# Kernel tuning notes

Hardware: AMD Instinct MI355X
Metric: run time of the kernel (lower is better)

## Reference

```python
import jax, jax.numpy as jnp
import numpy as np

NUM_CLASSES = 21
THRESH = 0.5
VAR = (0.1, 0.2)
B, P, O = 128, 8732, 16

def setup_inputs() -> dict:
    key = jax.random.key(0)
    ks = jax.random.split(key, 7)
    loc_preds = jax.random.normal(ks[0], (B, P, 4), jnp.float32)
    score_preds = jax.random.normal(ks[1], (B, P, NUM_CLASSES), jnp.float32)
    # priors in center-size form (cx, cy, w, h)
    pc = jax.random.uniform(ks[2], (P, 2), minval=0.05, maxval=0.95)
    pwh = jax.random.uniform(ks[3], (P, 2), minval=0.05, maxval=0.4)
    priors = jnp.concatenate([pc, pwh], axis=1).astype(jnp.float32)
    # ground truth: valid point-form boxes + label in last column
    gc = jax.random.uniform(ks[4], (B, O, 2), minval=0.2, maxval=0.8)
    gwh = jax.random.uniform(ks[5], (B, O, 2), minval=0.05, maxval=0.3)
    boxes = jnp.concatenate([gc - gwh / 2, gc + gwh / 2], axis=-1)
    labels = jax.random.randint(ks[6], (B, O, 1), 1, NUM_CLASSES).astype(jnp.float32)
    gt_data = jnp.concatenate([boxes, labels], axis=-1).astype(jnp.float32)
    return {"loc_preds": loc_preds, "score_preds": score_preds,
            "gt_data": gt_data, "priors": priors}

def _iou(a, b):
    # a: (O,4) point form, b: (P,4) point form -> (O,P)
    lt = jnp.maximum(a[:, None, :2], b[None, :, :2])
    rb = jnp.minimum(a[:, None, 2:], b[None, :, 2:])
    wh = jnp.clip(rb - lt, 0.0)
    inter = wh[..., 0] * wh[..., 1]
    area_a = (a[:, 2] - a[:, 0]) * (a[:, 3] - a[:, 1])
    area_b = (b[:, 2] - b[:, 0]) * (b[:, 3] - b[:, 1])
    return inter / (area_a[:, None] + area_b[None, :] - inter)

def _encode(matched, priors):
    # matched: (P,4) point form; priors: (P,4) center-size form
    g_c = (matched[:, :2] + matched[:, 2:]) / 2 - priors[:, :2]
    g_c = g_c / (VAR[0] * priors[:, 2:])
    g_wh = (matched[:, 2:] - matched[:, :2]) / priors[:, 2:]
    g_wh = jnp.log(g_wh) / VAR[1]
    return jnp.concatenate([g_c, g_wh], axis=1)

def _match_one(gt_loc, gt_cls, priors_pt, priors):
    ious = _iou(gt_loc, priors_pt)                    # (O, P)
    best_prior_idx = jnp.argmax(ious, axis=1)         # (O,)
    best_truth_overlap = jnp.max(ious, axis=0)        # (P,)
    best_truth_idx = jnp.argmax(ious, axis=0)         # (P,)
    # ensure every gt's best prior is kept positive and assigned to that gt
    best_truth_overlap = best_truth_overlap.at[best_prior_idx].set(2.0)
    best_truth_idx = best_truth_idx.at[best_prior_idx].set(jnp.arange(gt_loc.shape[0]))
    matched = gt_loc[best_truth_idx]                  # (P, 4)
    conf = gt_cls[best_truth_idx]
    conf = jnp.where(best_truth_overlap < THRESH, 0.0, conf)
    return _encode(matched, priors), conf.astype(jnp.int32)

def reference(loc_preds, score_preds, gt_data, priors):
    priors_pt = jnp.concatenate([priors[:, :2] - priors[:, 2:] / 2,
                                 priors[:, :2] + priors[:, 2:] / 2], axis=1)
    gt_loc, gt_cls = gt_data[..., :4], gt_data[..., 4]
    loc_targets, score_targets = jax.vmap(
        lambda l, c: _match_one(l, c, priors_pt, priors))(gt_loc, gt_cls)
    pos = score_targets > 0                           # (B, P)
    num_matched = jnp.sum(pos).astype(jnp.float32)

    # SmoothL1 over positive boxes (sum reduction)
    d = jnp.abs(loc_preds - loc_targets)
    sl1 = jnp.where(d < 1.0, 0.5 * d * d, d - 0.5)    # (B, P, 4)
    loc_loss = jnp.sum(jnp.where(pos[..., None], sl1, 0.0))

    # per-box cross-entropy on all boxes
    lse = jax.nn.logsumexp(score_preds, axis=-1)      # (B, P)
    gathered = jnp.take_along_axis(score_preds, score_targets[..., None],
                                   axis=-1)[..., 0]
    ce = lse - gathered                               # (B, P)

    # hard negative mining via double argsort ranking
    mine = jnp.where(pos, 0.0, ce)
    idx = jnp.argsort(-mine, axis=1)
    rank = jnp.argsort(idx, axis=1)
    num_pos = jnp.sum(pos, axis=1)                    # (B,)
    total_pos = jnp.sum(num_pos)
    num_neg = jnp.minimum(3 * num_pos, P - total_pos - 1)
    neg = rank < num_neg[:, None]

    sel = pos | neg
    conf_loss = jnp.sum(jnp.where(sel, ce, 0.0))
    return loc_loss / num_matched, conf_loss / num_matched
```

## Files before the change

### kernel.cpp

```cpp
#include <hip/hip_runtime.h>
#include <cstdint>
#include <cstddef>

#define B 128
#define P 8732
#define NC 21
#define O 16
#define THRESH 0.5f
#define NB1 8
#define NBX2 4
#define BPB 2304
#define WPW 576
#define NPART (B * NBX2)
#define SLABF 1536

typedef unsigned long long u64;
typedef unsigned int u32;
typedef unsigned char u8;

__device__ __forceinline__ float iou_pt(float a0, float a1, float a2, float a3,
                                        float b0, float b1, float b2, float b3) {
    float ltx = fmaxf(a0, b0), lty = fmaxf(a1, b1);
    float rbx = fminf(a2, b2), rby = fminf(a3, b3);
    float wx = fmaxf(rbx - ltx, 0.0f), wy = fmaxf(rby - lty, 0.0f);
    float inter = wx * wy;
    float aa = (a2 - a0) * (a3 - a1);
    float ab = (b2 - b0) * (b3 - b1);
    return inter / (aa + ab - inter);
}

__global__ void __launch_bounds__(256) k_pass1(const float* __restrict__ gt,
                                               const float* __restrict__ priors,
                                               u64* __restrict__ bk,
                                               u8* __restrict__ bidx) {
    const int b = blockIdx.y;
    __shared__ float s_gt[O * 4];
    __shared__ u64 s_wk[4][O];
    const int tid = threadIdx.x;
    const int wave = tid >> 6, lane = tid & 63;
    if (tid < O * 4) {
        int o = tid >> 2, c = tid & 3;
        s_gt[tid] = gt[(b * O + o) * 5 + c];
    }
    __syncthreads();

    u64 lk[O];
#pragma unroll
    for (int o = 0; o < O; o++) lk[o] = 0ull;

    for (int p = blockIdx.x * 256 + tid; p < P; p += NB1 * 256) {
        float4 pr = reinterpret_cast<const float4*>(priors)[p];
        float b0 = pr.x - pr.z * 0.5f, b1 = pr.y - pr.w * 0.5f;
        float b2 = pr.x + pr.z * 0.5f, b3 = pr.y + pr.w * 0.5f;
        float bov = -1.0f; int bo = 0;
#pragma unroll
        for (int o = 0; o < O; o++) {
            float v = iou_pt(s_gt[o * 4 + 0], s_gt[o * 4 + 1], s_gt[o * 4 + 2], s_gt[o * 4 + 3],
                             b0, b1, b2, b3);
            u64 key = ((u64)__float_as_uint(v) << 32) | (u64)(0xFFFFFFFFu - (u32)p);
            lk[o] = (key > lk[o]) ? key : lk[o];
            if (v > bov) { bov = v; bo = o; }
        }
        bidx[(size_t)b * P + p] = (u8)(bo | ((bov >= THRESH) ? 0x80 : 0));
    }

#pragma unroll
    for (int o = 0; o < O; o++) {
        u64 k = lk[o];
#pragma unroll
        for (int off = 32; off > 0; off >>= 1) {
            u64 other = (u64)__shfl_xor((long long)k, off, 64);
            k = (other > k) ? other : k;
        }
        if (lane == 0) s_wk[wave][o] = k;
    }
    __syncthreads();
    if (tid < O) {
        u64 k = s_wk[0][tid];
#pragma unroll
        for (int w = 1; w < 4; w++) { u64 v = s_wk[w][tid]; k = (v > k) ? v : k; }
        bk[((size_t)b * O + tid) * NB1 + blockIdx.x] = k;
    }
}

__device__ __forceinline__ void stage64(const float* __restrict__ gsrc,
                                        float* lds, int nf4, int lane) {
    const char* src = (const char*)gsrc;
    char* dst = (char*)lds;
#pragma unroll
    for (int i = 0; i < 6; i++) {
        int idx = i * 64 + lane;
        if (idx >= nf4) idx = nf4 - 1;
        __builtin_amdgcn_global_load_lds(
            (const __attribute__((address_space(1))) u32*)(src + (size_t)idx * 16),
            (__attribute__((address_space(3))) u32*)(dst + i * 1024),
            16, 0, 0);
    }
}

__global__ void __launch_bounds__(256) k_pass2(const float* __restrict__ gt,
                                               const float* __restrict__ priors,
                                               const u64* __restrict__ bk,
                                               const u8* __restrict__ bidx,
                                               const float* __restrict__ loc_preds,
                                               const float* __restrict__ scores,
                                               float* __restrict__ mine,
                                               double* __restrict__ pl,
                                               double* __restrict__ pc,
                                               int* __restrict__ pn) {
    const int b = blockIdx.y;
    const int tid = threadIdx.x;
    const int wave = tid >> 6, lane = tid & 63;
    __shared__ float s_slab[4][3][SLABF];
    __shared__ float s_gt[O * 5];
    __shared__ int s_bp[O];

    if (tid < O * 5) s_gt[tid] = gt[b * O * 5 + tid];
    if (tid < O) {
        u64 k = bk[((size_t)b * O + tid) * NB1];
#pragma unroll
        for (int i = 1; i < NB1; i++) {
            u64 v = bk[((size_t)b * O + tid) * NB1 + i];
            k = (v > k) ? v : k;
        }
        s_bp[tid] = (int)(0xFFFFFFFFu - (u32)(k & 0xFFFFFFFFull));
    }
    __syncthreads();

    const int wbase = blockIdx.x * BPB + wave * WPW;
    int wp = P - wbase; if (wp > WPW) wp = WPW;
    const int nchunk = (wp > 0) ? ((wp + 63) >> 6) : 0;

    float l_loc = 0.f, l_ce = 0.f;
    int l_np = 0;

    if (nchunk > 0) {
        for (int c0 = 0; c0 < 3 && c0 < nchunk; ++c0) {
            int nv0 = wp - c0 * 64; if (nv0 > 64) nv0 = 64;
            stage64(scores + ((size_t)b * P + wbase + c0 * 64) * NC,
                    &s_slab[wave][c0][0], nv0 * 21 / 4, lane);
        }
        for (int c = 0; c < nchunk; ++c) {
            const int base = wbase + c * 64;
            int nv = wp - c * 64; if (nv > 64) nv = 64;

            int ahead = nchunk - 1 - c; if (ahead > 2) ahead = 2;
            if (ahead == 2)      asm volatile("s_waitcnt vmcnt(12)" ::: "memory");
            else if (ahead == 1) asm volatile("s_waitcnt vmcnt(6)" ::: "memory");
            else                 asm volatile("s_waitcnt vmcnt(0)" ::: "memory");
            __builtin_amdgcn_sched_barrier(0);

            if (lane < nv) {
                const int p = base + lane;
                const float* fsl = &s_slab[wave][c % 3][lane * NC];
                float fs[NC];
#pragma unroll
                for (int cc = 0; cc < NC; cc++) fs[cc] = fsl[cc];

                int e = (int)bidx[(size_t)b * P + p];
                int best_idx = e & 0x3F;
                bool matched = (e & 0x80) != 0;
#pragma unroll
                for (int o = 0; o < O; o++) {
                    if (s_bp[o] == p) { best_idx = o; matched = true; }
                }
                int cls = matched ? (int)s_gt[best_idx * 5 + 4] : 0;

                float mx = fs[0];
#pragma unroll
                for (int cc = 1; cc < NC; cc++) mx = fmaxf(mx, fs[cc]);
                float se = 0.0f;
#pragma unroll
                for (int cc = 0; cc < NC; cc++) se += __expf(fs[cc] - mx);
                float lse = mx + __logf(se);
                float g = fs[0];
#pragma unroll
                for (int cc = 1; cc < NC; cc++) g = (cc == cls) ? fs[cc] : g;
                float ce = lse - g;

                mine[(size_t)b * P + p] = matched ? 0.0f : ce;

                if (matched) {
                    l_np++;
                    l_ce += ce;
                    float4 pr = reinterpret_cast<const float4*>(priors)[p];
                    float m0 = s_gt[best_idx * 5 + 0], m1 = s_gt[best_idx * 5 + 1];
                    float m2 = s_gt[best_idx * 5 + 2], m3 = s_gt[best_idx * 5 + 3];
                    float tx = ((m0 + m2) * 0.5f - pr.x) / (0.1f * pr.z);
                    float ty = ((m1 + m3) * 0.5f - pr.y) / (0.1f * pr.w);
                    float tw = __logf((m2 - m0) / pr.z) * 5.0f;
                    float th = __logf((m3 - m1) / pr.w) * 5.0f;
                    float4 lp = reinterpret_cast<const float4*>(loc_preds)[(size_t)b * P + p];
                    float d0 = fabsf(lp.x - tx), d1 = fabsf(lp.y - ty);
                    float d2 = fabsf(lp.z - tw), d3 = fabsf(lp.w - th);
                    float s0 = d0 < 1.0f ? 0.5f * d0 * d0 : d0 - 0.5f;
                    float s1 = d1 < 1.0f ? 0.5f * d1 * d1 : d1 - 0.5f;
                    float s2 = d2 < 1.0f ? 0.5f * d2 * d2 : d2 - 0.5f;
                    float s3 = d3 < 1.0f ? 0.5f * d3 * d3 : d3 - 0.5f;
                    l_loc += (s0 + s1) + (s2 + s3);
                }
            }

            if (c + 3 < nchunk) {
                int nv3 = wp - (c + 3) * 64; if (nv3 > 64) nv3 = 64;
                asm volatile("s_waitcnt lgkmcnt(0)" ::: "memory");
                stage64(scores + ((size_t)b * P + base + 3 * 64) * NC,
                        &s_slab[wave][c % 3][0], nv3 * 21 / 4, lane);
            }
        }
    }

#pragma unroll
    for (int off = 32; off > 0; off >>= 1) {
        l_loc += __shfl_xor(l_loc, off, 64);
        l_ce  += __shfl_xor(l_ce, off, 64);
        l_np  += __shfl_xor(l_np, off, 64);
    }
    __shared__ double s_loc[4], s_ce[4];
    __shared__ int s_np[4];
    if (lane == 0) { s_loc[wave] = (double)l_loc; s_ce[wave] = (double)l_ce; s_np[wave] = l_np; }
    __syncthreads();
    if (tid == 0) {
        int q = b * NBX2 + blockIdx.x;
        pl[q] = (s_loc[0] + s_loc[1]) + (s_loc[2] + s_loc[3]);
        pc[q] = (s_ce[0] + s_ce[1]) + (s_ce[2] + s_ce[3]);
        pn[q] = s_np[0] + s_np[1] + s_np[2] + s_np[3];
    }
}

__global__ void __launch_bounds__(1024) k_hardneg(const float* __restrict__ mine,
                                                  const int* __restrict__ pn,
                                                  double* __restrict__ pneg) {
    const int b = blockIdx.x;
    const int tid = threadIdx.x;
    const int lane = tid & 63, wave = tid >> 6;
    __shared__ float s_mine[P];
    __shared__ u32 s_hist[256];
    __shared__ u32 s_sel[2];
    __shared__ double s_red[16];
    __shared__ int s_ti[16];
    __shared__ int s_npx[NBX2];
    __shared__ int s_k;

    {
        int t = 0;
        for (int i = tid; i < NPART; i += 1024) t += pn[i];
#pragma unroll
        for (int off = 32; off > 0; off >>= 1) t += __shfl_xor(t, off, 64);
        if (lane == 0) s_ti[wave] = t;
    }
    if (tid < NBX2) s_npx[tid] = pn[b * NBX2 + tid];
    __syncthreads();
    if (tid == 0) {
        int tp = 0;
#pragma unroll
        for (int w = 0; w < 16; w++) tp += s_ti[w];
        int np = 0;
#pragma unroll
        for (int x = 0; x < NBX2; x++) np += s_npx[x];
        int k = 3 * np;
        int cap = P - tp - 1;
        if (cap < k) k = cap;
        s_k = k;
    }
    __syncthreads();
    const int k = s_k;

    if (k <= 0) {
        if (tid == 0) pneg[b] = 0.0;
        return;
    }

    for (int i = tid; i < P; i += 1024) s_mine[i] = mine[(size_t)b * P + i];
    if (tid == 0) { s_sel[0] = 0u; s_sel[1] = (u32)k; }
    __syncthreads();

    for (int shift = 24; shift >= 0; shift -= 8) {
        if (tid < 256) s_hist[tid] = 0u;
        __syncthreads();
        u32 prefix = s_sel[0];
        u32 kr = s_sel[1];
        u32 himask = (shift == 24) ? 0u : (0xFFFFFFFFu << (shift + 8));
        for (int i = tid; i < P; i += 1024) {
            u32 v = __float_as_uint(s_mine[i]);
            if ((v & himask) == prefix) atomicAdd(&s_hist[(v >> shift) & 255u], 1u);
        }
        __syncthreads();
        if (tid < 64) {
            const int L = tid;
            const int btop = 255 - 4 * L;
            u32 h0 = s_hist[btop], h1 = s_hist[btop - 1], h2 = s_hist[btop - 2], h3 = s_hist[btop - 3];
            u32 g4 = h0 + h1 + h2 + h3;
            u32 x = g4;
#pragma unroll
            for (int off = 1; off < 64; off <<= 1) {
                u32 v = __shfl_up(x, off, 64);
                if (L >= off) x += v;
            }
            u32 excl = x - g4;
            if (excl < kr && excl + g4 >= kr) {
                u32 c = excl; int chosen = btop; u32 kloc = kr;
                u32 nc;
                nc = c + h0; if (c < kr && nc >= kr) { chosen = btop;     kloc = kr - c; } c = nc;
                nc = c + h1; if (c < kr && nc >= kr) { chosen = btop - 1; kloc = kr - c; } c = nc;
                nc = c + h2; if (c < kr && nc >= kr) { chosen = btop - 2; kloc = kr - c; } c = nc;
                nc = c + h3; if (c < kr && nc >= kr) { chosen = btop - 3; kloc = kr - c; } c = nc;
                s_sel[0] = prefix | ((u32)chosen << shift);
                s_sel[1] = kloc;
            }
        }
        __syncthreads();
    }

    u32 tbits = s_sel[0];
    u32 kr = s_sel[1];
    float T = __uint_as_float(tbits);

    double sd = 0.0;
    for (int i = tid; i < P; i += 1024) {
        u32 v = __float_as_uint(s_mine[i]);
        if (v > tbits) sd += (double)s_mine[i];
    }
#pragma unroll
    for (int off = 32; off > 0; off >>= 1) sd += __shfl_xor(sd, off, 64);
    if (lane == 0) s_red[wave] = sd;
    __syncthreads();
    if (tid == 0) {
        double tt = 0.0;
#pragma unroll
        for (int w = 0; w < 16; w++) tt += s_red[w];
        pneg[b] = tt + (double)kr * (double)T;
    }
}

__global__ void __launch_bounds__(1024) k_fin(const double* __restrict__ pl,
                                              const double* __restrict__ pc,
                                              const int* __restrict__ pn,
                                              const double* __restrict__ pneg,
                                              float* __restrict__ out) {
    const int tid = threadIdx.x;
    const int lane = tid & 63, wave = tid >> 6;
    __shared__ double s_l[16], s_c[16], s_g[16];
    __shared__ int s_t[16];

    double tl = 0.0, tc = 0.0, tg = 0.0;
    int tn = 0;
    for (int i = tid; i < NPART; i += 1024) { tl += pl[i]; tc += pc[i]; tn += pn[i]; }
    if (tid < B) tg = pneg[tid];
#pragma unroll
    for (int off = 32; off > 0; off >>= 1) {
        tl += __shfl_xor(tl, off, 64);
        tc += __shfl_xor(tc, off, 64);
        tg += __shfl_xor(tg, off, 64);
        tn += __shfl_xor(tn, off, 64);
    }
    if (lane == 0) { s_l[wave] = tl; s_c[wave] = tc; s_g[wave] = tg; s_t[wave] = tn; }
    __syncthreads();
    if (tid == 0) {
        double al = 0.0, ac = 0.0, ag = 0.0;
        int an = 0;
#pragma unroll
        for (int w = 0; w < 16; w++) { al += s_l[w]; ac += s_c[w]; ag += s_g[w]; an += s_t[w]; }
        double n = (double)an;
        out[0] = (float)(al / n);
        out[1] = (float)((ac + ag) / n);
    }
}

extern "C" void kernel_launch(void* const* d_in, const int* in_sizes, int n_in,
                              void* d_out, int out_size, void* d_ws, size_t ws_size,
                              hipStream_t stream) {
    const float* loc_preds = (const float*)d_in[0];
    const float* scores    = (const float*)d_in[1];
    const float* gt        = (const float*)d_in[2];
    const float* priors    = (const float*)d_in[3];

    char* ws = (char*)d_ws;
    u64* bk      = (u64*)ws;
    double* pl   = (double*)(ws + 131072);
    double* pc   = (double*)(ws + 135168);
    int* pn      = (int*)(ws + 139264);
    double* pneg = (double*)(ws + 141312);
    u8* bidx     = (u8*)(ws + 142336);
    float* mine  = (float*)(ws + 1260032);


    k_pass1<<<dim3(NB1, B), dim3(256), 0, stream>>>(gt, priors, bk, bidx);
    k_pass2<<<dim3(NBX2, B), dim3(256), 0, stream>>>(
        gt, priors, bk, bidx, loc_preds, scores, mine, pl, pc, pn);
    k_hardneg<<<dim3(B), dim3(1024), 0, stream>>>(mine, pn, pneg);
    k_fin<<<dim3(1), dim3(1024), 0, stream>>>(pl, pc, pn, pneg, (float*)d_out);
}
```

Baseline: 60.99 us.

## Merge IoU matching and score streaming into one launch, fix positives separately

```diff
diff --git a/kernel.cpp b/kernel.cpp
--- a/kernel.cpp
+++ b/kernel.cpp
@@ -11,12 +11,15 @@
 #define NBX2 4
 #define BPB 2304
 #define WPW 576
-#define NPART (B * NBX2)
 #define SLABF 1536
+#define SCORE_BLKS (B * NBX2)
+#define P1_BLKS (B * NB1)
 
 typedef unsigned long long u64;
 typedef unsigned int u32;
 typedef unsigned char u8;
+
+#define VMW(n) asm volatile("s_waitcnt vmcnt(" #n ")" ::: "memory")
 
 __device__ __forceinline__ float iou_pt(float a0, float a1, float a2, float a3,
                                         float b0, float b1, float b2, float b3) {
@@ -29,60 +32,6 @@
     return inter / (aa + ab - inter);
 }
 
-__global__ void __launch_bounds__(256) k_pass1(const float* __restrict__ gt,
-                                               const float* __restrict__ priors,
-                                               u64* __restrict__ bk,
-                                               u8* __restrict__ bidx) {
-    const int b = blockIdx.y;
-    __shared__ float s_gt[O * 4];
-    __shared__ u64 s_wk[4][O];
-    const int tid = threadIdx.x;
-    const int wave = tid >> 6, lane = tid & 63;
-    if (tid < O * 4) {
-        int o = tid >> 2, c = tid & 3;
-        s_gt[tid] = gt[(b * O + o) * 5 + c];
-    }
-    __syncthreads();
-
-    u64 lk[O];
-#pragma unroll
-    for (int o = 0; o < O; o++) lk[o] = 0ull;
-
-    for (int p = blockIdx.x * 256 + tid; p < P; p += NB1 * 256) {
-        float4 pr = reinterpret_cast<const float4*>(priors)[p];
-        float b0 = pr.x - pr.z * 0.5f, b1 = pr.y - pr.w * 0.5f;
-        float b2 = pr.x + pr.z * 0.5f, b3 = pr.y + pr.w * 0.5f;
-        float bov = -1.0f; int bo = 0;
-#pragma unroll
-        for (int o = 0; o < O; o++) {
-            float v = iou_pt(s_gt[o * 4 + 0], s_gt[o * 4 + 1], s_gt[o * 4 + 2], s_gt[o * 4 + 3],
-                             b0, b1, b2, b3);
-            u64 key = ((u64)__float_as_uint(v) << 32) | (u64)(0xFFFFFFFFu - (u32)p);
-            lk[o] = (key > lk[o]) ? key : lk[o];
-            if (v > bov) { bov = v; bo = o; }
-        }
-        bidx[(size_t)b * P + p] = (u8)(bo | ((bov >= THRESH) ? 0x80 : 0));
-    }
-
-#pragma unroll
-    for (int o = 0; o < O; o++) {
-        u64 k = lk[o];
-#pragma unroll
-        for (int off = 32; off > 0; off >>= 1) {
-            u64 other = (u64)__shfl_xor((long long)k, off, 64);
-            k = (other > k) ? other : k;
-        }
-        if (lane == 0) s_wk[wave][o] = k;
-    }
-    __syncthreads();
-    if (tid < O) {
-        u64 k = s_wk[0][tid];
-#pragma unroll
-        for (int w = 1; w < 4; w++) { u64 v = s_wk[w][tid]; k = (v > k) ? v : k; }
-        bk[((size_t)b * O + tid) * NB1 + blockIdx.x] = k;
-    }
-}
-
 __device__ __forceinline__ void stage64(const float* __restrict__ gsrc,
                                         float* lds, int nf4, int lane) {
     const char* src = (const char*)gsrc;
@@ -98,73 +47,50 @@
     }
 }
 
-__global__ void __launch_bounds__(256) k_pass2(const float* __restrict__ gt,
-                                               const float* __restrict__ priors,
-                                               const u64* __restrict__ bk,
-                                               const u8* __restrict__ bidx,
-                                               const float* __restrict__ loc_preds,
-                                               const float* __restrict__ scores,
-                                               float* __restrict__ mine,
-                                               double* __restrict__ pl,
-                                               double* __restrict__ pc,
-                                               int* __restrict__ pn) {
-    const int b = blockIdx.y;
+__global__ void __launch_bounds__(256) k_main(const float* __restrict__ gt,
+                                              const float* __restrict__ priors,
+                                              const float* __restrict__ scores,
+                                              u64* __restrict__ bk,
+                                              u8* __restrict__ bidx,
+                                              float* __restrict__ mine) {
+    __shared__ union {
+        float slab[4][3][SLABF];
+        struct { u64 wk[4][O]; float gt4[O * 4]; } p1;
+    } sm;
     const int tid = threadIdx.x;
     const int wave = tid >> 6, lane = tid & 63;
-    __shared__ float s_slab[4][3][SLABF];
-    __shared__ float s_gt[O * 5];
-    __shared__ int s_bp[O];
-
-    if (tid < O * 5) s_gt[tid] = gt[b * O * 5 + tid];
-    if (tid < O) {
-        u64 k = bk[((size_t)b * O + tid) * NB1];
-#pragma unroll
-        for (int i = 1; i < NB1; i++) {
-            u64 v = bk[((size_t)b * O + tid) * NB1 + i];
-            k = (v > k) ? v : k;
-        }
-        s_bp[tid] = (int)(0xFFFFFFFFu - (u32)(k & 0xFFFFFFFFull));
-    }
-    __syncthreads();
-
-    const int wbase = blockIdx.x * BPB + wave * WPW;
-    int wp = P - wbase; if (wp > WPW) wp = WPW;
-    const int nchunk = (wp > 0) ? ((wp + 63) >> 6) : 0;
-
-    float l_loc = 0.f, l_ce = 0.f;
-    int l_np = 0;
-
-    if (nchunk > 0) {
+    const int bid = blockIdx.x;
+
+    if (bid < SCORE_BLKS) {
+        const int b = bid >> 2;
+        const int bx = bid & 3;
+        const int wbase = bx * BPB + wave * WPW;
+        int wp = P - wbase; if (wp > WPW) wp = WPW;
+        const int nchunk = (wp + 63) >> 6;
+
         for (int c0 = 0; c0 < 3 && c0 < nchunk; ++c0) {
             int nv0 = wp - c0 * 64; if (nv0 > 64) nv0 = 64;
             stage64(scores + ((size_t)b * P + wbase + c0 * 64) * NC,
-                    &s_slab[wave][c0][0], nv0 * 21 / 4, lane);
+                    &sm.slab[wave][c0][0], nv0 * 21 / 4, lane);
         }
         for (int c = 0; c < nchunk; ++c) {
             const int base = wbase + c * 64;
             int nv = wp - c * 64; if (nv > 64) nv = 64;
-
             int ahead = nchunk - 1 - c; if (ahead > 2) ahead = 2;
-            if (ahead == 2)      asm volatile("s_waitcnt vmcnt(12)" ::: "memory");
-            else if (ahead == 1) asm volatile("s_waitcnt vmcnt(6)" ::: "memory");
-            else                 asm volatile("s_waitcnt vmcnt(0)" ::: "memory");
+            if (ahead == 2) {
+                if (c == 0) VMW(12); else if (c == 1) VMW(13); else VMW(14);
+            } else if (ahead == 1) {
+                if (c == 0) VMW(6); else if (c == 1) VMW(7); else VMW(8);
+            } else {
+                VMW(0);
+            }
             __builtin_amdgcn_sched_barrier(0);
 
             if (lane < nv) {
-                const int p = base + lane;
-                const float* fsl = &s_slab[wave][c % 3][lane * NC];
+                const float* fsl = &sm.slab[wave][c % 3][lane * NC];
                 float fs[NC];
 #pragma unroll
                 for (int cc = 0; cc < NC; cc++) fs[cc] = fsl[cc];
-
-                int e = (int)bidx[(size_t)b * P + p];
-                int best_idx = e & 0x3F;
-                bool matched = (e & 0x80) != 0;
-#pragma unroll
-                for (int o = 0; o < O; o++) {
-                    if (s_bp[o] == p) { best_idx = o; matched = true; }
-                }
-                int cls = matched ? (int)s_gt[best_idx * 5 + 4] : 0;
 
                 float mx = fs[0];
 #pragma unroll
@@ -173,39 +99,151 @@
 #pragma unroll
                 for (int cc = 0; cc < NC; cc++) se += __expf(fs[cc] - mx);
                 float lse = mx + __logf(se);
-                float g = fs[0];
-#pragma unroll
-                for (int cc = 1; cc < NC; cc++) g = (cc == cls) ? fs[cc] : g;
-                float ce = lse - g;
-
-                mine[(size_t)b * P + p] = matched ? 0.0f : ce;
-
-                if (matched) {
-                    l_np++;
-                    l_ce += ce;
-                    float4 pr = reinterpret_cast<const float4*>(priors)[p];
-                    float m0 = s_gt[best_idx * 5 + 0], m1 = s_gt[best_idx * 5 + 1];
-                    float m2 = s_gt[best_idx * 5 + 2], m3 = s_gt[best_idx * 5 + 3];
-                    float tx = ((m0 + m2) * 0.5f - pr.x) / (0.1f * pr.z);
-                    float ty = ((m1 + m3) * 0.5f - pr.y) / (0.1f * pr.w);
-                    float tw = __logf((m2 - m0) / pr.z) * 5.0f;
-                    float th = __logf((m3 - m1) / pr.w) * 5.0f;
-                    float4 lp = reinterpret_cast<const float4*>(loc_preds)[(size_t)b * P + p];
-                    float d0 = fabsf(lp.x - tx), d1 = fabsf(lp.y - ty);
-                    float d2 = fabsf(lp.z - tw), d3 = fabsf(lp.w - th);
-                    float s0 = d0 < 1.0f ? 0.5f * d0 * d0 : d0 - 0.5f;
-                    float s1 = d1 < 1.0f ? 0.5f * d1 * d1 : d1 - 0.5f;
-                    float s2 = d2 < 1.0f ? 0.5f * d2 * d2 : d2 - 0.5f;
-                    float s3 = d3 < 1.0f ? 0.5f * d3 * d3 : d3 - 0.5f;
-                    l_loc += (s0 + s1) + (s2 + s3);
-                }
+                mine[(size_t)b * P + base + lane] = lse - fs[0];
             }
 
             if (c + 3 < nchunk) {
                 int nv3 = wp - (c + 3) * 64; if (nv3 > 64) nv3 = 64;
                 asm volatile("s_waitcnt lgkmcnt(0)" ::: "memory");
                 stage64(scores + ((size_t)b * P + base + 3 * 64) * NC,
-                        &s_slab[wave][c % 3][0], nv3 * 21 / 4, lane);
+                        &sm.slab[wave][c % 3][0], nv3 * 21 / 4, lane);
+            }
+        }
+    } else {
+        const int pid = bid - SCORE_BLKS;
+        const int bx = pid & 7;
+        const int b = pid >> 3;
+        if (tid < O * 4) {
+            int o = tid >> 2, c = tid & 3;
+            sm.p1.gt4[tid] = gt[(b * O + o) * 5 + c];
+        }
+        __syncthreads();
+
+        u64 lk[O];
+#pragma unroll
+        for (int o = 0; o < O; o++) lk[o] = 0ull;
+
+        for (int p = bx * 256 + tid; p < P; p += NB1 * 256) {
+            float4 pr = reinterpret_cast<const float4*>(priors)[p];
+            float b0 = pr.x - pr.z * 0.5f, b1 = pr.y - pr.w * 0.5f;
+            float b2 = pr.x + pr.z * 0.5f, b3 = pr.y + pr.w * 0.5f;
+            float bov = -1.0f; int bo = 0;
+#pragma unroll
+            for (int o = 0; o < O; o++) {
+                float v = iou_pt(sm.p1.gt4[o * 4 + 0], sm.p1.gt4[o * 4 + 1],
+                                 sm.p1.gt4[o * 4 + 2], sm.p1.gt4[o * 4 + 3],
+                                 b0, b1, b2, b3);
+                u64 key = ((u64)__float_as_uint(v) << 32) | (u64)(0xFFFFFFFFu - (u32)p);
+                lk[o] = (key > lk[o]) ? key : lk[o];
+                if (v > bov) { bov = v; bo = o; }
+            }
+            bidx[(size_t)b * P + p] = (u8)(bo | ((bov >= THRESH) ? 0x80 : 0));
+        }
+
+#pragma unroll
+        for (int o = 0; o < O; o++) {
+            u64 k = lk[o];
+#pragma unroll
+            for (int off = 32; off > 0; off >>= 1) {
+                u64 other = (u64)__shfl_xor((long long)k, off, 64);
+                k = (other > k) ? other : k;
+            }
+            if (lane == 0) sm.p1.wk[wave][o] = k;
+        }
+        __syncthreads();
+        if (tid < O) {
+            u64 k = sm.p1.wk[0][tid];
+#pragma unroll
+            for (int w = 1; w < 4; w++) { u64 v = sm.p1.wk[w][tid]; k = (v > k) ? v : k; }
+            bk[((size_t)b * O + tid) * NB1 + bx] = k;
+        }
+    }
+}
+
+__global__ void __launch_bounds__(256) k_fix(const float* __restrict__ gt,
+                                             const float* __restrict__ priors,
+                                             const float* __restrict__ loc_preds,
+                                             const float* __restrict__ scores,
+                                             const u64* __restrict__ bk,
+                                             const u8* __restrict__ bidx,
+                                             float* __restrict__ mine,
+                                             int* __restrict__ npA,
+                                             double* __restrict__ plA,
+                                             double* __restrict__ pcA,
+                                             double* __restrict__ acc,
+                                             u32* __restrict__ ticket) {
+    const int b = blockIdx.x;
+    const int tid = threadIdx.x;
+    const int lane = tid & 63, wave = tid >> 6;
+    __shared__ float s_gt[O * 5];
+    __shared__ int s_ovr[O];
+    __shared__ double s_l[4], s_c[4];
+    __shared__ int s_n[4];
+
+    if (b == 0 && tid == 0) { acc[0] = 0.0; *ticket = 0u; }
+    if (tid < O * 5) s_gt[tid] = gt[b * O * 5 + tid];
+    if (tid < O) {
+        u64 k = bk[((size_t)b * O + tid) * NB1];
+#pragma unroll
+        for (int i = 1; i < NB1; i++) {
+            u64 v = bk[((size_t)b * O + tid) * NB1 + i];
+            k = (v > k) ? v : k;
+        }
+        s_ovr[tid] = (int)(0xFFFFFFFFu - (u32)(k & 0xFFFFFFFFull));
+    }
+    __syncthreads();
+
+    float l_loc = 0.f, l_ce = 0.f;
+    int l_np = 0;
+
+    for (int i4 = tid; i4 < P / 4; i4 += 256) {
+        u32 w = *reinterpret_cast<const u32*>(bidx + (size_t)b * P + i4 * 4);
+#pragma unroll
+        for (int j = 0; j < 4; j++) {
+            const int p = i4 * 4 + j;
+            int e = (int)((w >> (8 * j)) & 0xFFu);
+#pragma unroll
+            for (int o = 0; o < O; o++)
+                if (s_ovr[o] == p) e = o | 0x80;
+            if (e & 0x80) {
+                int best_idx = e & 0x3F;
+                int cls = (int)s_gt[best_idx * 5 + 4];
+
+                const float* sp = scores + ((size_t)b * P + p) * NC;
+                float fs[NC];
+#pragma unroll
+                for (int cc = 0; cc < NC; cc++) fs[cc] = sp[cc];
+                float mx = fs[0];
+#pragma unroll
+                for (int cc = 1; cc < NC; cc++) mx = fmaxf(mx, fs[cc]);
+                float se = 0.0f;
+#pragma unroll
+                for (int cc = 0; cc < NC; cc++) se += __expf(fs[cc] - mx);
+                float lse = mx + __logf(se);
+                float g = fs[0];
+#pragma unroll
+                for (int cc = 1; cc < NC; cc++) g = (cc == cls) ? fs[cc] : g;
+                float ce = lse - g;
+
+                mine[(size_t)b * P + p] = 0.0f;
+                l_np++;
+                l_ce += ce;
+
+                float4 pr = reinterpret_cast<const float4*>(priors)[p];
+                float m0 = s_gt[best_idx * 5 + 0], m1 = s_gt[best_idx * 5 + 1];
+                float m2 = s_gt[best_idx * 5 + 2], m3 = s_gt[best_idx * 5 + 3];
+                float tx = ((m0 + m2) * 0.5f - pr.x) / (0.1f * pr.z);
+                float ty = ((m1 + m3) * 0.5f - pr.y) / (0.1f * pr.w);
+                float tw = __logf((m2 - m0) / pr.z) * 5.0f;
+                float th = __logf((m3 - m1) / pr.w) * 5.0f;
+                float4 lp = reinterpret_cast<const float4*>(loc_preds)[(size_t)b * P + p];
+                float d0 = fabsf(lp.x - tx), d1 = fabsf(lp.y - ty);
+                float d2 = fabsf(lp.z - tw), d3 = fabsf(lp.w - th);
+                float s0 = d0 < 1.0f ? 0.5f * d0 * d0 : d0 - 0.5f;
+                float s1 = d1 < 1.0f ? 0.5f * d1 * d1 : d1 - 0.5f;
+                float s2 = d2 < 1.0f ? 0.5f * d2 * d2 : d2 - 0.5f;
+                float s3 = d3 < 1.0f ? 0.5f * d3 * d3 : d3 - 0.5f;
+                l_loc += (s0 + s1) + (s2 + s3);
             }
         }
     }
@@ -216,21 +254,22 @@
         l_ce  += __shfl_xor(l_ce, off, 64);
         l_np  += __shfl_xor(l_np, off, 64);
     }
-    __shared__ double s_loc[4], s_ce[4];
-    __shared__ int s_np[4];
-    if (lane == 0) { s_loc[wave] = (double)l_loc; s_ce[wave] = (double)l_ce; s_np[wave] = l_np; }
+    if (lane == 0) { s_l[wave] = (double)l_loc; s_c[wave] = (double)l_ce; s_n[wave] = l_np; }
     __syncthreads();
     if (tid == 0) {
-        int q = b * NBX2 + blockIdx.x;
-        pl[q] = (s_loc[0] + s_loc[1]) + (s_loc[2] + s_loc[3]);
-        pc[q] = (s_ce[0] + s_ce[1]) + (s_ce[2] + s_ce[3]);
-        pn[q] = s_np[0] + s_np[1] + s_np[2] + s_np[3];
+        plA[b] = (s_l[0] + s_l[1]) + (s_l[2] + s_l[3]);
+        pcA[b] = (s_c[0] + s_c[1]) + (s_c[2] + s_c[3]);
+        npA[b] = s_n[0] + s_n[1] + s_n[2] + s_n[3];
     }
 }
 
 __global__ void __launch_bounds__(1024) k_hardneg(const float* __restrict__ mine,
-                                                  const int* __restrict__ pn,
-                                                  double* __restrict__ pneg) {
+                                                  const int* __restrict__ npA,
+                                                  const double* __restrict__ plA,
+                                                  const double* __restrict__ pcA,
+                                                  double* __restrict__ acc,
+                                                  u32* __restrict__ ticket,
+                                                  float* __restrict__ out) {
     const int b = blockIdx.x;
     const int tid = threadIdx.x;
     const int lane = tid & 63, wave = tid >> 6;
@@ -238,130 +277,95 @@
     __shared__ u32 s_hist[256];
     __shared__ u32 s_sel[2];
     __shared__ double s_red[16];
-    __shared__ int s_ti[16];
-    __shared__ int s_npx[NBX2];
-    __shared__ int s_k;
-
-    {
-        int t = 0;
-        for (int i = tid; i < NPART; i += 1024) t += pn[i];
-#pragma unroll
-        for (int off = 32; off > 0; off >>= 1) t += __shfl_xor(t, off, 64);
-        if (lane == 0) s_ti[wave] = t;
-    }
-    if (tid < NBX2) s_npx[tid] = pn[b * NBX2 + tid];
-    __syncthreads();
+    __shared__ int s_k, s_tp;
+
     if (tid == 0) {
         int tp = 0;
-#pragma unroll
-        for (int w = 0; w < 16; w++) tp += s_ti[w];
-        int np = 0;
-#pragma unroll
-        for (int x = 0; x < NBX2; x++) np += s_npx[x];
+        for (int i = 0; i < B; i++) tp += npA[i];
+        int np = npA[b];
         int k = 3 * np;
         int cap = P - tp - 1;
         if (cap < k) k = cap;
         s_k = k;
+        s_tp = tp;
     }
     __syncthreads();
     const int k = s_k;
 
-    if (k <= 0) {
-        if (tid == 0) pneg[b] = 0.0;
-        return;
-    }
-
-    for (int i = tid; i < P; i += 1024) s_mine[i] = mine[(size_t)b * P + i];
-    if (tid == 0) { s_sel[0] = 0u; s_sel[1] = (u32)k; }
-    __syncthreads();
-
-    for (int shift = 24; shift >= 0; shift -= 8) {
-        if (tid < 256) s_hist[tid] = 0u;
+    if (k > 0) {
+        for (int i = tid; i < P; i += 1024) s_mine[i] = mine[(size_t)b * P + i];
+        if (tid == 0) { s_sel[0] = 0u; s_sel[1] = (u32)k; }
         __syncthreads();
-        u32 prefix = s_sel[0];
+
+        for (int shift = 24; shift >= 0; shift -= 8) {
+            if (tid < 256) s_hist[tid] = 0u;
+            __syncthreads();
+            u32 prefix = s_sel[0];
+            u32 kr = s_sel[1];
+            u32 himask = (shift == 24) ? 0u : (0xFFFFFFFFu << (shift + 8));
+            for (int i = tid; i < P; i += 1024) {
+                u32 v = __float_as_uint(s_mine[i]);
+                if ((v & himask) == prefix) atomicAdd(&s_hist[(v >> shift) & 255u], 1u);
+            }
+            __syncthreads();
+            if (tid < 64) {
+                const int L = tid;
+                const int btop = 255 - 4 * L;
+                u32 h0 = s_hist[btop], h1 = s_hist[btop - 1], h2 = s_hist[btop - 2], h3 = s_hist[btop - 3];
+                u32 g4 = h0 + h1 + h2 + h3;
+                u32 x = g4;
+#pragma unroll
+                for (int off = 1; off < 64; off <<= 1) {
+                    u32 v = __shfl_up(x, off, 64);
+                    if (L >= off) x += v;
+                }
+                u32 excl = x - g4;
+                if (excl < kr && excl + g4 >= kr) {
+                    u32 c = excl; int chosen = btop; u32 kloc = kr;
+                    u32 nc;
+                    nc = c + h0; if (c < kr && nc >= kr) { chosen = btop;     kloc = kr - c; } c = nc;
+                    nc = c + h1; if (c < kr && nc >= kr) { chosen = btop - 1; kloc = kr - c; } c = nc;
+                    nc = c + h2; if (c < kr && nc >= kr) { chosen = btop - 2; kloc = kr - c; } c = nc;
+                    nc = c + h3; if (c < kr && nc >= kr) { chosen = btop - 3; kloc = kr - c; } c = nc;
+                    s_sel[0] = prefix | ((u32)chosen << shift);
+                    s_sel[1] = kloc;
+                }
+            }
+            __syncthreads();
+        }
+
+        u32 tbits = s_sel[0];
         u32 kr = s_sel[1];
-        u32 himask = (shift == 24) ? 0u : (0xFFFFFFFFu << (shift + 8));
+        float T = __uint_as_float(tbits);
+
+        double sd = 0.0;
         for (int i = tid; i < P; i += 1024) {
             u32 v = __float_as_uint(s_mine[i]);
-            if ((v & himask) == prefix) atomicAdd(&s_hist[(v >> shift) & 255u], 1u);
-        }
+            if (v > tbits) sd += (double)s_mine[i];
+        }
+#pragma unroll
+        for (int off = 32; off > 0; off >>= 1) sd += __shfl_xor(sd, off, 64);
+        if (lane == 0) s_red[wave] = sd;
         __syncthreads();
-        if (tid < 64) {
-            const int L = tid;
-            const int btop = 255 - 4 * L;
-            u32 h0 = s_hist[btop], h1 = s_hist[btop - 1], h2 = s_hist[btop - 2], h3 = s_hist[btop - 3];
-            u32 g4 = h0 + h1 + h2 + h3;
-            u32 x = g4;
-#pragma unroll
-            for (int off = 1; off < 64; off <<= 1) {
-                u32 v = __shfl_up(x, off, 64);
-                if (L >= off) x += v;
-            }
-            u32 excl = x - g4;
-            if (excl < kr && excl + g4 >= kr) {
-                u32 c = excl; int chosen = btop; u32 kloc = kr;
-                u32 nc;
-                nc = c + h0; if (c < kr && nc >= kr) { chosen = btop;     kloc = kr - c; } c = nc;
-                nc = c + h1; if (c < kr && nc >= kr) { chosen = btop - 1; kloc = kr - c; } c = nc;
-                nc = c + h2; if (c < kr && nc >= kr) { chosen = btop - 2; kloc = kr - c; } c = nc;
-                nc = c + h3; if (c < kr && nc >= kr) { chosen = btop - 3; kloc = kr - c; } c = nc;
-                s_sel[0] = prefix | ((u32)chosen << shift);
-                s_sel[1] = kloc;
-            }
-        }
-        __syncthreads();
-    }
-
-    u32 tbits = s_sel[0];
-    u32 kr = s_sel[1];
-    float T = __uint_as_float(tbits);
-
-    double sd = 0.0;
-    for (int i = tid; i < P; i += 1024) {
-        u32 v = __float_as_uint(s_mine[i]);
-        if (v > tbits) sd += (double)s_mine[i];
-    }
-#pragma unroll
-    for (int off = 32; off > 0; off >>= 1) sd += __shfl_xor(sd, off, 64);
-    if (lane == 0) s_red[wave] = sd;
-    __syncthreads();
-    if (tid == 0) {
-        double tt = 0.0;
-#pragma unroll
-        for (int w = 0; w < 16; w++) tt += s_red[w];
-        pneg[b] = tt + (double)kr * (double)T;
-    }
-}
-
-__global__ void __launch_bounds__(1024) k_fin(const double* __restrict__ pl,
-                                              const double* __restrict__ pc,
-                                              const int* __restrict__ pn,
-                                              const double* __restrict__ pneg,
-                                              float* __restrict__ out) {
-    const int tid = threadIdx.x;
-    const int lane = tid & 63, wave = tid >> 6;
-    __shared__ double s_l[16], s_c[16], s_g[16];
-    __shared__ int s_t[16];
-
-    double tl = 0.0, tc = 0.0, tg = 0.0;
-    int tn = 0;
-    for (int i = tid; i < NPART; i += 1024) { tl += pl[i]; tc += pc[i]; tn += pn[i]; }
-    if (tid < B) tg = pneg[tid];
-#pragma unroll
-    for (int off = 32; off > 0; off >>= 1) {
-        tl += __shfl_xor(tl, off, 64);
-        tc += __shfl_xor(tc, off, 64);
-        tg += __shfl_xor(tg, off, 64);
-        tn += __shfl_xor(tn, off, 64);
-    }
-    if (lane == 0) { s_l[wave] = tl; s_c[wave] = tc; s_g[wave] = tg; s_t[wave] = tn; }
-    __syncthreads();
-    if (tid == 0) {
-        double al = 0.0, ac = 0.0, ag = 0.0;
-        int an = 0;
-#pragma unroll
-        for (int w = 0; w < 16; w++) { al += s_l[w]; ac += s_c[w]; ag += s_g[w]; an += s_t[w]; }
-        double n = (double)an;
+        if (tid == 0) {
+            double tt = 0.0;
+#pragma unroll
+            for (int w = 0; w < 16; w++) tt += s_red[w];
+            atomicAdd(&acc[0], tt + (double)kr * (double)T);
+        }
+    }
+
+    __threadfence();
+    __syncthreads();
+    __shared__ int s_last;
+    if (tid == 0) s_last = (atomicAdd(ticket, 1u) == B - 1) ? 1 : 0;
+    __syncthreads();
+    if (s_last && tid == 0) {
+        double al = 0.0, ac = 0.0;
+        for (int i = 0; i < B; i++) { al += plA[i]; ac += pcA[i]; }
+        __threadfence();
+        double ag = atomicAdd(&acc[0], 0.0);
+        double n = (double)s_tp;
         out[0] = (float)(al / n);
         out[1] = (float)((ac + ag) / n);
     }
@@ -377,17 +381,19 @@
 
     char* ws = (char*)d_ws;
     u64* bk      = (u64*)ws;
-    double* pl   = (double*)(ws + 131072);
-    double* pc   = (double*)(ws + 135168);
-    int* pn      = (int*)(ws + 139264);
-    double* pneg = (double*)(ws + 141312);
-    u8* bidx     = (u8*)(ws + 142336);
-    float* mine  = (float*)(ws + 1260032);
-
-
-    k_pass1<<<dim3(NB1, B), dim3(256), 0, stream>>>(gt, priors, bk, bidx);
-    k_pass2<<<dim3(NBX2, B), dim3(256), 0, stream>>>(
-        gt, priors, bk, bidx, loc_preds, scores, mine, pl, pc, pn);
-    k_hardneg<<<dim3(B), dim3(1024), 0, stream>>>(mine, pn, pneg);
-    k_fin<<<dim3(1), dim3(1024), 0, stream>>>(pl, pc, pn, pneg, (float*)d_out);
-}
+    int* npA     = (int*)(ws + 131072);
+    double* plA  = (double*)(ws + 131584);
+    double* pcA  = (double*)(ws + 132608);
+    double* acc  = (double*)(ws + 133632);
+    u32* ticket  = (u32*)(ws + 133640);
+    u8* bidx     = (u8*)(ws + 133648);
+    float* mine  = (float*)(ws + 1251360);
+
+
+    k_main<<<dim3(SCORE_BLKS + P1_BLKS), dim3(256), 0, stream>>>(
+        gt, priors, scores, bk, bidx, mine);
+    k_fix<<<dim3(B), dim3(256), 0, stream>>>(
+        gt, priors, loc_preds, scores, bk, bidx, mine, npA, plA, pcA, acc, ticket);
+    k_hardneg<<<dim3(B), dim3(1024), 0, stream>>>(mine, npA, plA, pcA, acc, ticket,
+                                                  (float*)d_out);
+}
```

Result: slower. 146.2 us (+139.7%).
